# Kernel tuning notes

Hardware: AMD Instinct MI355X
Metric: run time of the kernel (lower is better)

The kernel has to match this reference:

```python
import jax, jax.numpy as jnp
import numpy as np
import math

B, T, DIM, NH, NKV, HD = 1, 2048, 1024, 16, 8, 64
N_REP = NH // NKV
LAMBDA_INIT = 0.8 - 0.6 * math.exp(-0.3)  # layer_idx = 0
EPS = 1e-5


def _rope(t, cos, sin):
    # t: (B, T, H, HD); cos/sin: (T, HD//2)
    tr = t.reshape(t.shape[:-1] + (HD // 2, 2))
    r, i = tr[..., 0], tr[..., 1]
    c = cos[None, :, None, :]
    s = sin[None, :, None, :]
    out_r = r * c - i * s
    out_i = r * s + i * c
    return jnp.stack([out_r, out_i], axis=-1).reshape(t.shape)


def setup_inputs():
    key = jax.random.key(0)
    ks = jax.random.split(key, 9)
    x = jax.random.normal(ks[0], (B, T, DIM), jnp.float32)
    inv_freq = 1.0 / (10000.0 ** (np.arange(0, HD, 2, dtype=np.float32) / HD))
    angles = np.outer(np.arange(T, dtype=np.float32), inv_freq)  # (T, HD//2)
    freqs_cos = jnp.asarray(np.cos(angles), jnp.float32)
    freqs_sin = jnp.asarray(np.sin(angles), jnp.float32)
    wq = jax.random.normal(ks[1], (2 * NH * HD, DIM), jnp.float32) * 0.02
    wk = jax.random.normal(ks[2], (2 * NKV * HD, DIM), jnp.float32) * 0.02
    wv = jax.random.normal(ks[3], (NKV * HD, DIM), jnp.float32) * 0.02
    wo = jax.random.normal(ks[4], (DIM, NH * HD), jnp.float32) * 0.02
    lambda_q1 = jax.random.normal(ks[5], (HD,), jnp.float32) * 0.1
    lambda_k1 = jax.random.normal(ks[6], (HD,), jnp.float32) * 0.1
    lambda_q2 = jax.random.normal(ks[7], (HD,), jnp.float32) * 0.1
    lambda_k2 = jax.random.normal(ks[8], (HD,), jnp.float32) * 0.1
    return dict(x=x, freqs_cos=freqs_cos, freqs_sin=freqs_sin, wq=wq, wk=wk,
                wv=wv, wo=wo, lambda_q1=lambda_q1, lambda_k1=lambda_k1,
                lambda_q2=lambda_q2, lambda_k2=lambda_k2)


def reference(x, freqs_cos, freqs_sin, wq, wk, wv, wo,
              lambda_q1, lambda_k1, lambda_q2, lambda_k2):
    Bc, Tc, C = x.shape
    q = (x @ wq.T).reshape(Bc, Tc, NH, 2, HD)
    k = (x @ wk.T).reshape(Bc, Tc, NKV, 2, HD)
    v = (x @ wv.T).reshape(Bc, Tc, NKV, HD)
    q1, q2 = q[..., 0, :], q[..., 1, :]
    k1, k2 = k[..., 0, :], k[..., 1, :]
    q1 = _rope(q1, freqs_cos, freqs_sin)
    k1 = _rope(k1, freqs_cos, freqs_sin)
    q2 = _rope(q2, freqs_cos, freqs_sin)
    k2 = _rope(k2, freqs_cos, freqs_sin)
    # GQA: repeat each kv head n_rep times consecutively
    k1 = jnp.repeat(k1, N_REP, axis=2)
    k2 = jnp.repeat(k2, N_REP, axis=2)
    v = jnp.repeat(v, N_REP, axis=2)
    # (B, H, T, HD)
    q1, q2 = jnp.swapaxes(q1, 1, 2), jnp.swapaxes(q2, 1, 2)
    k1, k2 = jnp.swapaxes(k1, 1, 2), jnp.swapaxes(k2, 1, 2)
    v = jnp.swapaxes(v, 1, 2)
    scale = 1.0 / math.sqrt(HD)
    mask = jnp.tril(jnp.ones((Tc, Tc), bool))

    def attn_probs(qh, kh):
        s = jnp.einsum('bhtd,bhsd->bhts', qh, kh) * scale
        s = jnp.where(mask[None, None], s, -jnp.inf)
        return jax.nn.softmax(s, axis=-1)

    a1 = attn_probs(q1, k1)
    a2 = attn_probs(q2, k2)
    lam = (jnp.exp(jnp.sum(lambda_q1 * lambda_k1))
           - jnp.exp(jnp.sum(lambda_q2 * lambda_k2)) + LAMBDA_INIT)
    y = jnp.einsum('bhts,bhsd->bhtd', a1 - lam * a2, v)  # (B,H,T,HD)
    y = jnp.swapaxes(y, 1, 2)  # (B,T,H,HD)
    # GroupNorm(num_groups=NH, affine=False) on (B,C,T): normalize per (batch, head)
    # over (T, HD) elements.
    mean = y.mean(axis=(1, 3), keepdims=True)
    var = y.var(axis=(1, 3), keepdims=True)
    y = (y - mean) / jnp.sqrt(var + EPS)
    y = y.reshape(Bc, Tc, C) * (1.0 - LAMBDA_INIT)
    return y @ wo.T
```

## Files before the change

kernel.cpp:

```cpp
#include <hip/hip_runtime.h>
#include <hip/hip_bf16.h>
#include <cstdint>

#define T_SEQ 2048
#define DIM   1024
#define NHEAD 16
#define NKVH  8
#define HDIM  64
#define QKVN  3584

static constexpr float LAMBDA_INIT_F = 0.3555090675909693f;
static constexpr float ONE_MINUS_LI  = 0.6444909324090307f;
static constexpr float QSCALE_EXP2   = 0.1803368801111144f;

typedef __bf16 bf16x8 __attribute__((ext_vector_type(8)));
typedef float  f32x4  __attribute__((ext_vector_type(4)));

static __device__ __forceinline__ ushort f2bf(float f) {
  union { float f; uint32_t u; } x; x.f = f;
  uint32_t u = x.u;
  uint32_t r = (u + 0x7fffu + ((u >> 16) & 1u)) >> 16;
  return (ushort)r;
}
static __device__ __forceinline__ float bf2f(ushort u) {
  union { uint32_t u; float f; } x; x.u = ((uint32_t)u) << 16; return x.f;
}
static __device__ __forceinline__ f32x4 zero4() {
  f32x4 z = {0.f, 0.f, 0.f, 0.f}; return z;
}
static __device__ __forceinline__ bf16x8 ldfrag128(const ushort* p) {
  union { bf16x8 v; uint4 u; } r;
  r.u = *(const uint4*)p;
  return r.v;
}
static __device__ __forceinline__ void gll16(const ushort* g, ushort* l) {
  __builtin_amdgcn_global_load_lds(
      (const __attribute__((address_space(1))) uint32_t*)g,
      (__attribute__((address_space(3))) uint32_t*)l, 16, 0, 0);
}

__global__ void cvt_all(const float* __restrict__ x,  const float* __restrict__ wq,
                        const float* __restrict__ wk, const float* __restrict__ wv,
                        const float* __restrict__ wo,
                        ushort* __restrict__ xb, ushort* __restrict__ Wb,
                        ushort* __restrict__ Wob) {
  int g = (blockIdx.x * 256 + threadIdx.x) * 4;
  float4 v; ushort* dst; int j;
  if (g < 2097152) {
    v = *(const float4*)(x + g); dst = xb; j = g;
  } else if (g < 5767168) {
    j = g - 2097152;
    const float* src = (j < 2097152) ? (wq + j)
                     : (j < 3145728) ? (wk + (j - 2097152))
                                     : (wv + (j - 3145728));
    v = *(const float4*)src; dst = Wb;
  } else {
    j = g - 5767168;
    v = *(const float4*)(wo + j); dst = Wob;
  }
  int q = (j & 31) >> 2;
  int jp = (j & ~31) + ((q & 3) << 3) + ((q >> 2) << 2);
  ushort4 o4;
  o4.x = f2bf(v.x); o4.y = f2bf(v.y); o4.z = f2bf(v.z); o4.w = f2bf(v.w);
  *(ushort4*)(dst + jp) = o4;
}

__global__ void lam_kernel(const float* __restrict__ lq1, const float* __restrict__ lk1,
                           const float* __restrict__ lq2, const float* __restrict__ lk2,
                           float* __restrict__ lam) {
  int lane = threadIdx.x;
  float p1 = lq1[lane] * lk1[lane];
  float p2 = lq2[lane] * lk2[lane];
  #pragma unroll
  for (int off = 32; off >= 1; off >>= 1) {
    p1 += __shfl_down(p1, off);
    p2 += __shfl_down(p2, off);
  }
  if (lane == 0) *lam = expf(p1) - expf(p2) + LAMBDA_INIT_F;
}

template<int BF16OUT>
__global__ __launch_bounds__(256) void gemm_bt(const ushort* __restrict__ A,
                                               const ushort* __restrict__ W,
                                               void* __restrict__ Cout,
                                               int M, int N, int K) {
  __shared__ __align__(16) ushort As[2 * 128 * 32];
  __shared__ __align__(16) ushort Ws[2 * 128 * 32];
  const int tid  = threadIdx.x;
  const int lane = tid & 63;
  const int w    = tid >> 6;
  const int wr   = w >> 1, wc = w & 1;
  const int nwg = gridDim.x * gridDim.y;
  int id  = blockIdx.x * gridDim.y + blockIdx.y;
  int sw  = (id & 7) * (nwg >> 3) + (id >> 3);
  const int bm = (sw % gridDim.y) * 128;
  const int bn = (sw / gridDim.y) * 128;
  const int fr = lane & 15;
  const int fg = (lane >> 4) * 4;
  const int g8 = (lane >> 4) * 8;

  f32x4 acc[4][4];
  #pragma unroll
  for (int m = 0; m < 4; ++m)
    #pragma unroll
    for (int n = 0; n < 4; ++n) acc[m][n] = zero4();

  const int col  = (lane & 3) * 8;
  const int row0 = w * 16 + (lane >> 2);
  const int row1 = row0 + 64;
  const ushort* ga0 = A + (size_t)(bm + row0) * K + col;
  const ushort* ga1 = A + (size_t)(bm + row1) * K + col;
  const ushort* gw0 = W + (size_t)(bn + row0) * K + col;
  const ushort* gw1 = W + (size_t)(bn + row1) * K + col;
  ushort* la0 = As + (w * 512);
  ushort* la1 = As + (w * 512) + 2048;
  ushort* la2 = As + 4096 + (w * 512);
  ushort* la3 = As + 4096 + (w * 512) + 2048;
  ushort* lw0 = Ws + (w * 512);
  ushort* lw1 = Ws + (w * 512) + 2048;
  ushort* lw2 = Ws + 4096 + (w * 512);
  ushort* lw3 = Ws + 4096 + (w * 512) + 2048;

  for (int k0 = 0; k0 < K; k0 += 64) {
    gll16(ga0 + k0,      la0);
    gll16(ga1 + k0,      la1);
    gll16(ga0 + k0 + 32, la2);
    gll16(ga1 + k0 + 32, la3);
    gll16(gw0 + k0,      lw0);
    gll16(gw1 + k0,      lw1);
    gll16(gw0 + k0 + 32, lw2);
    gll16(gw1 + k0 + 32, lw3);
    __syncthreads();
    #pragma unroll
    for (int kk = 0; kk < 2; ++kk) {
      bf16x8 af[4], bfr[4];
      #pragma unroll
      for (int m = 0; m < 4; ++m)
        af[m]  = ldfrag128(&As[kk*4096 + (wr*64 + m*16 + fr) * 32 + g8]);
      #pragma unroll
      for (int n = 0; n < 4; ++n)
        bfr[n] = ldfrag128(&Ws[kk*4096 + (wc*64 + n*16 + fr) * 32 + g8]);
      #pragma unroll
      for (int m = 0; m < 4; ++m)
        #pragma unroll
        for (int n = 0; n < 4; ++n)
          acc[m][n] = __builtin_amdgcn_mfma_f32_16x16x32_bf16(af[m], bfr[n], acc[m][n], 0, 0, 0);
    }
    __syncthreads();
  }

  #pragma unroll
  for (int m = 0; m < 4; ++m)
    #pragma unroll
    for (int n = 0; n < 4; ++n)
      #pragma unroll
      for (int i = 0; i < 4; ++i) {
        int row = bm + wr*64 + m*16 + fg + i;
        int colg = bn + wc*64 + n*16 + fr;
        float v = acc[m][n][i];
        if (BF16OUT) ((ushort*)Cout)[(size_t)row * N + colg] = f2bf(v);
        else         ((float*)Cout)[(size_t)row * N + colg]  = v;
      }
}

__global__ void reorg(const ushort* __restrict__ QKV, ushort* __restrict__ Qr,
                      ushort* __restrict__ Kr, ushort* __restrict__ Vt,
                      const float* __restrict__ fc, const float* __restrict__ fs) {
  int idx = blockIdx.x * 256 + threadIdx.x;
  if (idx < 786432) {
    int nheads, col_off; ushort* dst; float scale; int id;
    if (idx < 524288) { id = idx * 4; nheads = NHEAD; col_off = 0; dst = Qr; scale = QSCALE_EXP2; }
    else { id = (idx - 524288) * 4; nheads = NKVH; col_off = 2048; dst = Kr; scale = 1.0f; }
    int per_t = nheads * 64;
    int t  = id / per_t;
    int r  = id - t * per_t;
    int hh = r >> 6;
    int c2 = (r >> 5) & 1;
    int j  = r & 31;
    int cl = col_off + hh * 128 + c2 * 64 + 2 * j;
    uint4 raw = *(const uint4*)(QKV + (size_t)t * QKVN + cl);
    const ushort* rp = (const ushort*)&raw;
    float c4[4], s4[4];
    *(float4*)c4 = *(const float4*)(fc + t * 32 + j);
    *(float4*)s4 = *(const float4*)(fs + t * 32 + j);
    ushort outv[8];
    #pragma unroll
    for (int p = 0; p < 4; ++p) {
      float rv = bf2f(rp[2*p]), iv = bf2f(rp[2*p + 1]);
      outv[2*p]     = f2bf((rv * c4[p] - iv * s4[p]) * scale);
      outv[2*p + 1] = f2bf((rv * s4[p] + iv * c4[p]) * scale);
    }
    int d0  = 2 * j;
    int ks  = (d0 >> 5) & 1;
    int dlo = d0 & 31;
    int gb  = (dlo >> 2) & 2;
    int e   = (dlo & 16) >> 2;
    size_t base = ((size_t)(c2 * nheads + hh) * T_SEQ + (t & ~15)) * HDIM
                + ks * 512 + (t & 15) * 8;
    *(uint2*)(dst + base + gb * 128 + e)        = *(const uint2*)(outv);
    *(uint2*)(dst + base + (gb + 1) * 128 + e)  = *(const uint2*)(outv + 4);
  } else {
    int id = (idx - 786432) * 8;
    int t = id & (T_SEQ - 1);
    int rest = id >> 11;
    int kh = rest >> 6, d = rest & 63;
    ushort outv[8];
    #pragma unroll
    for (int p = 0; p < 8; ++p) outv[p] = QKV[(size_t)(t + p) * QKVN + 3072 + rest];
    int tlo = t & 31;
    int gb  = (tlo >> 2) & 2;
    int e   = (tlo & 16) >> 2;
    size_t base = (size_t)kh * (64 * T_SEQ)
                + ((size_t)((t >> 5) * 4 + (d >> 4))) * 512 + (d & 15) * 8;
    *(uint2*)(Vt + base + gb * 128 + e)        = *(const uint2*)(outv);
    *(uint2*)(Vt + base + (gb + 1) * 128 + e)  = *(const uint2*)(outv + 4);
  }
}

__global__ __launch_bounds__(256, 2) void attn_kernel(const ushort* __restrict__ Qr,
                                                      const ushort* __restrict__ Kr,
                                                      const ushort* __restrict__ Vt,
                                                      const float* __restrict__ lamp,
                                                      float* __restrict__ Yf,
                                                      float* __restrict__ part) {
  const int bx = blockIdx.x;
  const int h  = bx & 15;
  const int jb = bx >> 4;
  const int qb = (jb < 16) ? (31 - jb) : (jb - 16);
  const int kh = h >> 1;
  const int tid = threadIdx.x;
  const int lane = tid & 63;
  const int w   = tid >> 6;
  const int st  = w >> 1;
  const int qh  = w & 1;
  const int fr  = lane & 15;
  const int fg  = (lane >> 4) * 4;

  __shared__ float ob[64 * 64];
  __shared__ float sb[8];

  bf16x8 qf[2][2];
  #pragma unroll
  for (int qs = 0; qs < 2; ++qs) {
    const ushort* qp = Qr + (size_t)(st * NHEAD + h) * (T_SEQ * HDIM)
                     + (size_t)(qb * 4 + qh * 2 + qs) * 1024 + lane * 8;
    qf[qs][0] = ldfrag128(qp);
    qf[qs][1] = ldfrag128(qp + 512);
  }

  float m_[2] = {-__builtin_inff(), -__builtin_inff()};
  float l_[2] = {0.f, 0.f};
  f32x4 o_[2][4];
  #pragma unroll
  for (int qs = 0; qs < 2; ++qs)
    #pragma unroll
    for (int dn = 0; dn < 4; ++dn) o_[qs][dn] = zero4();

  const ushort* Kbase = Kr + (size_t)(st * NKVH + kh) * (T_SEQ * HDIM) + lane * 8;
  const ushort* Vbase = Vt + (size_t)kh * (64 * T_SEQ) + lane * 8;

#define SINGLE_TILE(KT, DOMASK) do {                                          \
    bf16x8 kf_[4][2], vf_[4][2];                                              \
    _Pragma("unroll")                                                         \
    for (int n_ = 0; n_ < 4; ++n_) {                                          \
      const ushort* kp_ = Kbase + (size_t)((KT) * 4 + n_) * 1024;             \
      kf_[n_][0] = ldfrag128(kp_);                                            \
      kf_[n_][1] = ldfrag128(kp_ + 512);                                      \
    }                                                                         \
    _Pragma("unroll")                                                         \
    for (int ks_ = 0; ks_ < 2; ++ks_) {                                       \
      const ushort* vp_ = Vbase + (size_t)(((KT) * 2 + ks_) * 4) * 512;       \
      _Pragma("unroll")                                                       \
      for (int dn_ = 0; dn_ < 4; ++dn_)                                       \
        vf_[dn_][ks_] = ldfrag128(vp_ + dn_ * 512);                           \
    }                                                                         \
    float sv_[2][4][4];                                                       \
    __builtin_amdgcn_s_setprio(1);                                            \
    _Pragma("unroll")                                                         \
    for (int n_ = 0; n_ < 4; ++n_) {                                          \
      f32x4 a0_ = zero4(), a1_ = zero4();                                     \
      _Pragma("unroll")                                                       \
      for (int ks_ = 0; ks_ < 2; ++ks_) {                                     \
        a0_ = __builtin_amdgcn_mfma_f32_16x16x32_bf16(kf_[n_][ks_], qf[0][ks_], a0_, 0, 0, 0); \
        a1_ = __builtin_amdgcn_mfma_f32_16x16x32_bf16(kf_[n_][ks_], qf[1][ks_], a1_, 0, 0, 0); \
      }                                                                       \
      _Pragma("unroll")                                                       \
      for (int i_ = 0; i_ < 4; ++i_) { sv_[0][n_][i_] = a0_[i_]; sv_[1][n_][i_] = a1_[i_]; } \
    }                                                                         \
    __builtin_amdgcn_s_setprio(0);                                            \
    if (DOMASK) {                                                             \
      _Pragma("unroll")                                                       \
      for (int qs_ = 0; qs_ < 2; ++qs_) {                                     \
        const int qloc_ = qh*32 + qs_*16 + fr;                                \
        _Pragma("unroll")                                                     \
        for (int n_ = 0; n_ < 4; ++n_)                                        \
          _Pragma("unroll")                                                   \
          for (int i_ = 0; i_ < 4; ++i_)                                      \
            if (n_*16 + fg + i_ > qloc_) sv_[qs_][n_][i_] = -__builtin_inff();\
      }                                                                       \
    }                                                                         \
    bf16x8 pa_[2][2];                                                         \
    _Pragma("unroll")                                                         \
    for (int qs_ = 0; qs_ < 2; ++qs_) {                                       \
      float rm_ = -__builtin_inff();                                          \
      _Pragma("unroll")                                                       \
      for (int n_ = 0; n_ < 4; ++n_)                                          \
        _Pragma("unroll")                                                     \
        for (int i_ = 0; i_ < 4; ++i_) rm_ = fmaxf(rm_, sv_[qs_][n_][i_]);    \
      rm_ = fmaxf(rm_, __shfl_xor(rm_, 16));                                  \
      rm_ = fmaxf(rm_, __shfl_xor(rm_, 32));                                  \
      if (!__all(rm_ <= m_[qs_] + 8.f)) {                                     \
        float mnew_ = fmaxf(m_[qs_], rm_);                                    \
        float sc_ = __builtin_amdgcn_exp2f(m_[qs_] - mnew_);                  \
        m_[qs_] = mnew_;                                                      \
        l_[qs_] *= sc_;                                                       \
        float scs_[4];                                                        \
        _Pragma("unroll")                                                     \
        for (int i_ = 0; i_ < 4; ++i_) scs_[i_] = __shfl(sc_, fg + i_);       \
        _Pragma("unroll")                                                     \
        for (int dn_ = 0; dn_ < 4; ++dn_)                                     \
          _Pragma("unroll")                                                   \
          for (int i_ = 0; i_ < 4; ++i_) o_[qs_][dn_][i_] *= scs_[i_];        \
      }                                                                       \
      float rs_ = 0.f;                                                        \
      _Pragma("unroll")                                                       \
      for (int n_ = 0; n_ < 4; ++n_)                                          \
        _Pragma("unroll")                                                     \
        for (int i_ = 0; i_ < 4; ++i_) {                                      \
          float p_ = __builtin_amdgcn_exp2f(sv_[qs_][n_][i_] - m_[qs_]);      \
          sv_[qs_][n_][i_] = p_; rs_ += p_;                                   \
        }                                                                     \
      rs_ += __shfl_xor(rs_, 16);                                             \
      rs_ += __shfl_xor(rs_, 32);                                             \
      l_[qs_] += rs_;                                                         \
      _Pragma("unroll")                                                       \
      for (int ks_ = 0; ks_ < 2; ++ks_)                                       \
        _Pragma("unroll")                                                     \
        for (int n2_ = 0; n2_ < 2; ++n2_)                                     \
          _Pragma("unroll")                                                   \
          for (int i_ = 0; i_ < 4; ++i_)                                      \
            pa_[qs_][ks_][n2_*4 + i_] = (__bf16)sv_[qs_][2*ks_ + n2_][i_];    \
    }                                                                         \
    __builtin_amdgcn_s_setprio(1);                                            \
    _Pragma("unroll")                                                         \
    for (int ks_ = 0; ks_ < 2; ++ks_)                                         \
      _Pragma("unroll")                                                       \
      for (int dn_ = 0; dn_ < 4; ++dn_) {                                     \
        o_[0][dn_] = __builtin_amdgcn_mfma_f32_16x16x32_bf16(pa_[0][ks_], vf_[dn_][ks_], o_[0][dn_], 0, 0, 0); \
        o_[1][dn_] = __builtin_amdgcn_mfma_f32_16x16x32_bf16(pa_[1][ks_], vf_[dn_][ks_], o_[1][dn_], 0, 0, 0); \
      }                                                                       \
    __builtin_amdgcn_s_setprio(0);                                            \
  } while (0)

  const int nnd = qb;
  int kt = 0;
  for (; kt + 1 < nnd; kt += 2) {
    bf16x8 kfA[4][2], vfA[4][2], kfB[4][2], vfB[4][2];
    #pragma unroll
    for (int n = 0; n < 4; ++n) {
      const ushort* kpA = Kbase + (size_t)(kt * 4 + n) * 1024;
      const ushort* kpB = kpA + 4096;
      kfA[n][0] = ldfrag128(kpA);  kfA[n][1] = ldfrag128(kpA + 512);
      kfB[n][0] = ldfrag128(kpB);  kfB[n][1] = ldfrag128(kpB + 512);
    }
    #pragma unroll
    for (int ks = 0; ks < 2; ++ks) {
      const ushort* vpA = Vbase + (size_t)((kt * 2 + ks) * 4) * 512;
      const ushort* vpB = vpA + 4096;
      #pragma unroll
      for (int dn = 0; dn < 4; ++dn) {
        vfA[dn][ks] = ldfrag128(vpA + dn * 512);
        vfB[dn][ks] = ldfrag128(vpB + dn * 512);
      }
    }
    float svA[2][4][4], svB[2][4][4];
    __builtin_amdgcn_s_setprio(1);
    #pragma unroll
    for (int n = 0; n < 4; ++n) {
      f32x4 a0 = zero4(), a1 = zero4(), b0 = zero4(), b1 = zero4();
      #pragma unroll
      for (int ks = 0; ks < 2; ++ks) {
        a0 = __builtin_amdgcn_mfma_f32_16x16x32_bf16(kfA[n][ks], qf[0][ks], a0, 0, 0, 0);
        a1 = __builtin_amdgcn_mfma_f32_16x16x32_bf16(kfA[n][ks], qf[1][ks], a1, 0, 0, 0);
        b0 = __builtin_amdgcn_mfma_f32_16x16x32_bf16(kfB[n][ks], qf[0][ks], b0, 0, 0, 0);
        b1 = __builtin_amdgcn_mfma_f32_16x16x32_bf16(kfB[n][ks], qf[1][ks], b1, 0, 0, 0);
      }
      #pragma unroll
      for (int i = 0; i < 4; ++i) {
        svA[0][n][i] = a0[i]; svA[1][n][i] = a1[i];
        svB[0][n][i] = b0[i]; svB[1][n][i] = b1[i];
      }
    }
    __builtin_amdgcn_s_setprio(0);

    bf16x8 paA[2][2], paB[2][2];
    #pragma unroll
    for (int qs = 0; qs < 2; ++qs) {
      float rm = -__builtin_inff();
      #pragma unroll
      for (int n = 0; n < 4; ++n)
        #pragma unroll
        for (int i = 0; i < 4; ++i) {
          rm = fmaxf(rm, svA[qs][n][i]);
          rm = fmaxf(rm, svB[qs][n][i]);
        }
      rm = fmaxf(rm, __shfl_xor(rm, 16));
      rm = fmaxf(rm, __shfl_xor(rm, 32));
      if (!__all(rm <= m_[qs] + 8.f)) {
        float mnew = fmaxf(m_[qs], rm);
        float sc = __builtin_amdgcn_exp2f(m_[qs] - mnew);
        m_[qs] = mnew;
        l_[qs] *= sc;
        float scs[4];
        #pragma unroll
        for (int i = 0; i < 4; ++i) scs[i] = __shfl(sc, fg + i);
        #pragma unroll
        for (int dn = 0; dn < 4; ++dn)
          #pragma unroll
          for (int i = 0; i < 4; ++i) o_[qs][dn][i] *= scs[i];
      }
      float rs = 0.f;
      #pragma unroll
      for (int n = 0; n < 4; ++n)
        #pragma unroll
        for (int i = 0; i < 4; ++i) {
          float pA = __builtin_amdgcn_exp2f(svA[qs][n][i] - m_[qs]);
          float pB = __builtin_amdgcn_exp2f(svB[qs][n][i] - m_[qs]);
          svA[qs][n][i] = pA; svB[qs][n][i] = pB;
          rs += pA + pB;
        }
      rs += __shfl_xor(rs, 16);
      rs += __shfl_xor(rs, 32);
      l_[qs] += rs;
      #pragma unroll
      for (int ks = 0; ks < 2; ++ks)
        #pragma unroll
        for (int n2 = 0; n2 < 2; ++n2)
          #pragma unroll
          for (int i = 0; i < 4; ++i) {
            paA[qs][ks][n2*4 + i] = (__bf16)svA[qs][2*ks + n2][i];
            paB[qs][ks][n2*4 + i] = (__bf16)svB[qs][2*ks + n2][i];
          }
    }

    __builtin_amdgcn_s_setprio(1);
    #pragma unroll
    for (int ks = 0; ks < 2; ++ks)
      #pragma unroll
      for (int dn = 0; dn < 4; ++dn) {
        o_[0][dn] = __builtin_amdgcn_mfma_f32_16x16x32_bf16(paA[0][ks], vfA[dn][ks], o_[0][dn], 0, 0, 0);
        o_[1][dn] = __builtin_amdgcn_mfma_f32_16x16x32_bf16(paA[1][ks], vfA[dn][ks], o_[1][dn], 0, 0, 0);
      }
    #pragma unroll
    for (int ks = 0; ks < 2; ++ks)
      #pragma unroll
      for (int dn = 0; dn < 4; ++dn) {
        o_[0][dn] = __builtin_amdgcn_mfma_f32_16x16x32_bf16(paB[0][ks], vfB[dn][ks], o_[0][dn], 0, 0, 0);
        o_[1][dn] = __builtin_amdgcn_mfma_f32_16x16x32_bf16(paB[1][ks], vfB[dn][ks], o_[1][dn], 0, 0, 0);
      }
    __builtin_amdgcn_s_setprio(0);
  }
  if (kt < nnd) { SINGLE_TILE(kt, 0); ++kt; }
  SINGLE_TILE(qb, 1);
#undef SINGLE_TILE

  float iq[2][4];
  #pragma unroll
  for (int qs = 0; qs < 2; ++qs) {
    float inv = __builtin_amdgcn_rcpf(l_[qs]);
    #pragma unroll
    for (int i = 0; i < 4; ++i) iq[qs][i] = __shfl(inv, fg + i);
  }
  __syncthreads();
  if (st == 1) {
    #pragma unroll
    for (int qs = 0; qs < 2; ++qs)
      #pragma unroll
      for (int dn = 0; dn < 4; ++dn)
        #pragma unroll
        for (int i = 0; i < 4; ++i)
          ob[(qh*32 + qs*16 + fg + i)*64 + dn*16 + fr] = o_[qs][dn][i] * iq[qs][i];
  }
  __syncthreads();
  if (st == 0) {
    const float lam = *lamp;
    float s = 0.f, s2 = 0.f;
    #pragma unroll
    for (int qs = 0; qs < 2; ++qs)
      #pragma unroll
      for (int dn = 0; dn < 4; ++dn)
        #pragma unroll
        for (int i = 0; i < 4; ++i) {
          int r64 = qh*32 + qs*16 + fg + i;
          int d   = dn*16 + fr;
          float v = o_[qs][dn][i] * iq[qs][i] - lam * ob[r64*64 + d];
          Yf[(size_t)(qb*64 + r64) * DIM + h*64 + d] = v;
          s += v; s2 += v * v;
        }
    #pragma unroll
    for (int off = 1; off <= 32; off <<= 1) {
      s  += __shfl_xor(s, off);
      s2 += __shfl_xor(s2, off);
    }
    if (lane == 0) { sb[w] = s; sb[4 + w] = s2; }
  }
  __syncthreads();
  if (tid == 0) {
    part[bx]       = sb[0] + sb[1];
    part[512 + bx] = sb[4] + sb[5];
  }
}

__global__ void stats_final(const float* __restrict__ part, float* __restrict__ stat) {
  int hh = threadIdx.x;
  if (hh < 16) {
    float S = 0.f, S2 = 0.f;
    #pragma unroll
    for (int j = 0; j < 32; ++j) { S += part[j*16 + hh]; S2 += part[512 + j*16 + hh]; }
    const float N = (float)(T_SEQ * HDIM);
    float mean = S / N;
    float var  = S2 / N - mean * mean;
    stat[hh]      = mean;
    stat[16 + hh] = rsqrtf(var + 1e-5f);
  }
}

__global__ void norm_cvt(const float* __restrict__ Y, const float* __restrict__ stats,
                         ushort* __restrict__ Yb) {
  int idx = (blockIdx.x * 256 + threadIdx.x) * 4;
  int col = idx & (DIM - 1);
  int h = col >> 6;
  float mean = stats[h], isd = stats[16 + h] * ONE_MINUS_LI;
  float4 v = *(const float4*)(Y + idx);
  ushort4 o4;
  o4.x = f2bf((v.x - mean) * isd);
  o4.y = f2bf((v.y - mean) * isd);
  o4.z = f2bf((v.z - mean) * isd);
  o4.w = f2bf((v.w - mean) * isd);
  int q = (col & 31) >> 2;
  int idxp = (idx & ~31) + ((q & 3) << 3) + ((q >> 2) << 2);
  *(ushort4*)(Yb + idxp) = o4;
}

extern "C" void kernel_launch(void* const* d_in, const int* in_sizes, int n_in,
                              void* d_out, int out_size, void* d_ws, size_t ws_size,
                              hipStream_t stream) {
  const float* x   = (const float*)d_in[0];
  const float* fc  = (const float*)d_in[1];
  const float* fs  = (const float*)d_in[2];
  const float* wq  = (const float*)d_in[3];
  const float* wk  = (const float*)d_in[4];
  const float* wv  = (const float*)d_in[5];
  const float* wo  = (const float*)d_in[6];
  const float* lq1 = (const float*)d_in[7];
  const float* lk1 = (const float*)d_in[8];
  const float* lq2 = (const float*)d_in[9];
  const float* lk2 = (const float*)d_in[10];
  float* out = (float*)d_out;

  char* ws = (char*)d_ws;
  const size_t OFF_WOB  = 0;
  const size_t OFF_XB   = 2097152;
  const size_t OFF_WB   = 6291456;
  const size_t OFF_QKV  = 13631488;
  const size_t OFF_QR   = 28311552;
  const size_t OFF_KR   = 36700160;
  const size_t OFF_VT   = 40894464;
  const size_t OFF_Y    = 18874368;
  const size_t OFF_YB   = 42991616;
  const size_t OFF_ST   = 47185920;

  ushort* xb   = (ushort*)(ws + OFF_XB);
  ushort* Wb   = (ushort*)(ws + OFF_WB);
  ushort* Wob  = (ushort*)(ws + OFF_WOB);
  ushort* QKVb = (ushort*)(ws + OFF_QKV);
  ushort* Qr   = (ushort*)(ws + OFF_QR);
  ushort* Kr   = (ushort*)(ws + OFF_KR);
  ushort* Vt   = (ushort*)(ws + OFF_VT);
  float*  Yf   = (float*)(ws + OFF_Y);
  ushort* Yb   = (ushort*)(ws + OFF_YB);
  float*  stat = (float*)(ws + OFF_ST);
  float*  lamp = stat + 32;
  float*  part = stat + 64;

  cvt_all<<<6656, 256, 0, stream>>>(x, wq, wk, wv, wo, xb, Wb, Wob);
  lam_kernel<<<1, 64, 0, stream>>>(lq1, lk1, lq2, lk2, lamp);

  gemm_bt<1><<<dim3(QKVN/128, T_SEQ/128), 256, 0, stream>>>(xb, Wb, QKVb, T_SEQ, QKVN, DIM);

  reorg<<<3584, 256, 0, stream>>>(QKVb, Qr, Kr, Vt, fc, fs);

  attn_kernel<<<512, 256, 0, stream>>>(Qr, Kr, Vt, lamp, Yf, part);

  stats_final<<<1, 64, 0, stream>>>(part, stat);
  norm_cvt<<<2048, 256, 0, stream>>>(Yf, stat, Yb);

  gemm_bt<0><<<dim3(DIM/128, T_SEQ/128), 256, 0, stream>>>(Yb, Wob, out, T_SEQ, DIM, DIM);
}
```

Baseline: 117.4 us.

## Split long causal query blocks across two KV-range workgroups and merge partials

The upper 16 query blocks, which have the longest causal KV ranges, are now split into two workgroups, each covering half of the KV tiles. Each writes unnormalized partial O along with row max and sum to a workspace buffer. A new merge_stats kernel combines the two halves with log-sum-exp rescaling, applies the lambda difference, and writes Y plus the GroupNorm partial sums. The aim is better load balance and more blocks across the CUs (768 instead of 512), at the cost of extra global traffic for the partials, one more kernel launch, and removal of the 2-blocks-per-CU launch bound.

```diff
diff --git a/kernel.cpp b/kernel.cpp
--- a/kernel.cpp
+++ b/kernel.cpp
@@ -217,17 +217,30 @@
   }
 }
 
-__global__ __launch_bounds__(256, 2) void attn_kernel(const ushort* __restrict__ Qr,
-                                                      const ushort* __restrict__ Kr,
-                                                      const ushort* __restrict__ Vt,
-                                                      const float* __restrict__ lamp,
-                                                      float* __restrict__ Yf,
-                                                      float* __restrict__ part) {
+__global__ __launch_bounds__(256) void attn_kernel(const ushort* __restrict__ Qr,
+                                                   const ushort* __restrict__ Kr,
+                                                   const ushort* __restrict__ Vt,
+                                                   const float* __restrict__ lamp,
+                                                   float* __restrict__ Yf,
+                                                   float* __restrict__ part,
+                                                   float* __restrict__ Opart,
+                                                   float* __restrict__ Ml) {
   const int bx = blockIdx.x;
-  const int h  = bx & 15;
-  const int jb = bx >> 4;
-  const int qb = (jb < 16) ? (31 - jb) : (jb - 16);
-  const int kh = h >> 1;
+  const int kh = bx & 7;
+  const int inner = bx >> 3;
+  const int h  = kh * 2 + (inner & 1);
+  const int s  = inner >> 1;
+  int qb, kt0, kt1, c;
+  if (s < 32) {
+    qb = 31 - (s >> 1); c = s & 1;
+    int sp = (qb + 1) >> 1;
+    kt0 = c ? sp : 0;
+    kt1 = c ? (qb + 1) : sp;
+  } else {
+    qb = 47 - s; c = -1;
+    kt0 = 0; kt1 = qb + 1;
+  }
+  const bool diag = (kt1 == qb + 1);
   const int tid = threadIdx.x;
   const int lane = tid & 63;
   const int w   = tid >> 6;
@@ -352,9 +365,9 @@
     __builtin_amdgcn_s_setprio(0);                                            \
   } while (0)
 
-  const int nnd = qb;
-  int kt = 0;
-  for (; kt + 1 < nnd; kt += 2) {
+  const int nomask_end = diag ? qb : kt1;
+  int kt = kt0;
+  for (; kt + 1 < nomask_end; kt += 2) {
     bf16x8 kfA[4][2], vfA[4][2], kfB[4][2], vfB[4][2];
     #pragma unroll
     for (int n = 0; n < 4; ++n) {
@@ -460,9 +473,32 @@
       }
     __builtin_amdgcn_s_setprio(0);
   }
-  if (kt < nnd) { SINGLE_TILE(kt, 0); ++kt; }
-  SINGLE_TILE(qb, 1);
+  if (kt < nomask_end) { SINGLE_TILE(kt, 0); ++kt; }
+  if (diag) SINGLE_TILE(qb, 1);
 #undef SINGLE_TILE
+
+  if (s < 32) {
+    const int plane = (c*2 + st)*16 + h;
+    #pragma unroll
+    for (int qs = 0; qs < 2; ++qs) {
+      float* op = Opart + (size_t)plane * 65536
+                + (size_t)((qb - 16) * 4 + qh * 2 + qs) * 1024 + lane;
+      #pragma unroll
+      for (int dn = 0; dn < 4; ++dn)
+        #pragma unroll
+        for (int i = 0; i < 4; ++i)
+          op[(dn*4 + i) * 64] = o_[qs][dn][i];
+    }
+    if (lane < 16) {
+      #pragma unroll
+      for (int qs = 0; qs < 2; ++qs) {
+        int rp = (qb - 16)*64 + qh*32 + qs*16 + fr;
+        Ml[(size_t)plane*1024 + rp]         = m_[qs];
+        Ml[65536 + (size_t)plane*1024 + rp] = l_[qs];
+      }
+    }
+    return;
+  }
 
   float iq[2][4];
   #pragma unroll
@@ -484,7 +520,7 @@
   __syncthreads();
   if (st == 0) {
     const float lam = *lamp;
-    float s = 0.f, s2 = 0.f;
+    float sa = 0.f, sa2 = 0.f;
     #pragma unroll
     for (int qs = 0; qs < 2; ++qs)
       #pragma unroll
@@ -495,19 +531,71 @@
           int d   = dn*16 + fr;
           float v = o_[qs][dn][i] * iq[qs][i] - lam * ob[r64*64 + d];
           Yf[(size_t)(qb*64 + r64) * DIM + h*64 + d] = v;
-          s += v; s2 += v * v;
+          sa += v; sa2 += v * v;
         }
     #pragma unroll
     for (int off = 1; off <= 32; off <<= 1) {
-      s  += __shfl_xor(s, off);
-      s2 += __shfl_xor(s2, off);
-    }
-    if (lane == 0) { sb[w] = s; sb[4 + w] = s2; }
+      sa  += __shfl_xor(sa, off);
+      sa2 += __shfl_xor(sa2, off);
+    }
+    if (lane == 0) { sb[w] = sa; sb[4 + w] = sa2; }
   }
   __syncthreads();
   if (tid == 0) {
-    part[bx]       = sb[0] + sb[1];
-    part[512 + bx] = sb[4] + sb[5];
+    part[qb*16 + h]       = sb[0] + sb[1];
+    part[512 + qb*16 + h] = sb[4] + sb[5];
+  }
+}
+
+__global__ __launch_bounds__(256) void merge_stats(const float* __restrict__ Opart,
+                                                   const float* __restrict__ Ml,
+                                                   const float* __restrict__ lamp,
+                                                   float* __restrict__ Yf,
+                                                   float* __restrict__ part) {
+  const int h = blockIdx.x & 15, sl = blockIdx.x >> 4;
+  const float lam = *lamp;
+  float s = 0.f, s2 = 0.f;
+  for (int e = threadIdx.x; e < 1024; e += 256) {
+    int rp = sl * 64 + (e >> 4);
+    int d4 = (e & 15) * 4;
+    int off = (rp >> 4) * 1024 + ((d4 >> 4) * 4 + (rp & 3)) * 64
+            + ((rp & 15) >> 2) * 16 + (d4 & 15);
+    float o[2][4];
+    #pragma unroll
+    for (int st = 0; st < 2; ++st) {
+      int p0 = st*16 + h;
+      int p1 = (2 + st)*16 + h;
+      float m0 = Ml[(size_t)p0*1024 + rp], l0 = Ml[65536 + (size_t)p0*1024 + rp];
+      float m1 = Ml[(size_t)p1*1024 + rp], l1 = Ml[65536 + (size_t)p1*1024 + rp];
+      float M  = fmaxf(m0, m1);
+      float w0 = __builtin_amdgcn_exp2f(m0 - M);
+      float w1 = __builtin_amdgcn_exp2f(m1 - M);
+      float inv = 1.f / (l0 * w0 + l1 * w1);
+      float4 a = *(const float4*)(Opart + (size_t)p0*65536 + off);
+      float4 b = *(const float4*)(Opart + (size_t)p1*65536 + off);
+      o[st][0] = (a.x * w0 + b.x * w1) * inv;
+      o[st][1] = (a.y * w0 + b.y * w1) * inv;
+      o[st][2] = (a.z * w0 + b.z * w1) * inv;
+      o[st][3] = (a.w * w0 + b.w * w1) * inv;
+    }
+    float4 v;
+    v.x = o[0][0] - lam * o[1][0];
+    v.y = o[0][1] - lam * o[1][1];
+    v.z = o[0][2] - lam * o[1][2];
+    v.w = o[0][3] - lam * o[1][3];
+    s  += v.x + v.y + v.z + v.w;
+    s2 += v.x*v.x + v.y*v.y + v.z*v.z + v.w*v.w;
+    *(float4*)(Yf + (size_t)(1024 + rp) * DIM + h * 64 + d4) = v;
+  }
+  #pragma unroll
+  for (int off = 32; off >= 1; off >>= 1) { s += __shfl_down(s, off); s2 += __shfl_down(s2, off); }
+  __shared__ float sb[8];
+  int wv = threadIdx.x >> 6, lane = threadIdx.x & 63;
+  if (lane == 0) { sb[wv] = s; sb[4 + wv] = s2; }
+  __syncthreads();
+  if (threadIdx.x == 0) {
+    part[256 + blockIdx.x]       = sb[0] + sb[1] + sb[2] + sb[3];
+    part[512 + 256 + blockIdx.x] = sb[4] + sb[5] + sb[6] + sb[7];
   }
 }
 
@@ -516,7 +604,10 @@
   if (hh < 16) {
     float S = 0.f, S2 = 0.f;
     #pragma unroll
-    for (int j = 0; j < 32; ++j) { S += part[j*16 + hh]; S2 += part[512 + j*16 + hh]; }
+    for (int j = 0; j < 16; ++j) {
+      S  += part[j*16 + hh] + part[256 + j*16 + hh];
+      S2 += part[512 + j*16 + hh] + part[512 + 256 + j*16 + hh];
+    }
     const float N = (float)(T_SEQ * HDIM);
     float mean = S / N;
     float var  = S2 / N - mean * mean;
@@ -566,7 +657,9 @@
   const size_t OFF_QR   = 28311552;
   const size_t OFF_KR   = 36700160;
   const size_t OFF_VT   = 40894464;
-  const size_t OFF_Y    = 18874368;
+  const size_t OFF_OP   = 2097152;
+  const size_t OFF_ML   = 18874368;
+  const size_t OFF_Y    = 19398656;
   const size_t OFF_YB   = 42991616;
   const size_t OFF_ST   = 47185920;
 
@@ -577,6 +670,8 @@
   ushort* Qr   = (ushort*)(ws + OFF_QR);
   ushort* Kr   = (ushort*)(ws + OFF_KR);
   ushort* Vt   = (ushort*)(ws + OFF_VT);
+  float*  Opart= (float*)(ws + OFF_OP);
+  float*  Ml   = (float*)(ws + OFF_ML);
   float*  Yf   = (float*)(ws + OFF_Y);
   ushort* Yb   = (ushort*)(ws + OFF_YB);
   float*  stat = (float*)(ws + OFF_ST);
@@ -590,8 +685,9 @@
 
   reorg<<<3584, 256, 0, stream>>>(QKVb, Qr, Kr, Vt, fc, fs);
 
-  attn_kernel<<<512, 256, 0, stream>>>(Qr, Kr, Vt, lamp, Yf, part);
-
+  attn_kernel<<<768, 256, 0, stream>>>(Qr, Kr, Vt, lamp, Yf, part, Opart, Ml);
+
+  merge_stats<<<256, 256, 0, stream>>>(Opart, Ml, lamp, Yf, part);
   stats_final<<<1, 64, 0, stream>>>(part, stat);
   norm_cvt<<<2048, 256, 0, stream>>>(Yf, stat, Yb);
 
```

After: 140.8 us. 1.2x slower.
